# Performance work log

Hardware: AMD Instinct MI355X
Metric: run time of the kernel (lower is better)

Reference implementation:

```python
import jax, jax.numpy as jnp
import numpy as np

T, B, I, H = 512, 64, 256, 256
ACT_EXP2 = 7   # activation scale = 2^-7
W_EXP2 = 8     # weight scale = 2^-8
QMIN, QMAX = -128.0, 127.0  # int8 symmetric, zp=0


def fq(x, exp2_inv):
    """Fake-quantize (round/clamp/dequant) with straight-through estimator."""
    scale = 2.0 ** (-exp2_inv)
    y = jnp.clip(jnp.round(x / scale), QMIN, QMAX) * scale
    return x + jax.lax.stop_gradient(y - x)


def setup_inputs() -> dict:
    key = jax.random.key(0)
    k = jax.random.split(key, 5)
    x = jax.random.normal(k[0], (T, B, I), jnp.float32)
    h0 = jnp.zeros((B, H), jnp.float32)
    W = jax.random.normal(k[1], (I, 3 * H), jnp.float32) / np.sqrt(I)
    R = jax.random.normal(k[2], (H, 3 * H), jnp.float32) / np.sqrt(H)
    bx = jax.random.normal(k[3], (3 * H,), jnp.float32) * 0.1
    br = jax.random.normal(k[4], (3 * H,), jnp.float32) * 0.1
    return {"x": x, "h0": h0, "W": W, "R": R, "bx": bx, "br": br}


def gru_quant(x, h0, W, R, bx, br):
    # quantize weights/biases once (weight.W / weight.R / weight.bx / weight.br)
    Wq = fq(W, W_EXP2)
    Rq = fq(R, W_EXP2)
    bxq = fq(bx, W_EXP2)
    brq = fq(br, W_EXP2)
    # hoisted input matmul: Wx = fq(fq(x) @ Wq)  -> [T, B, 3H]
    Wx = fq(jnp.einsum('tbi,ij->tbj', fq(x, ACT_EXP2), Wq), ACT_EXP2)
    Hh = h0.shape[-1]
    bz, brg, bg = bxq[:Hh], bxq[Hh:2 * Hh], bxq[2 * Hh:]

    def step(h, wx_t):
        hq = fq(h, ACT_EXP2)                      # input.h
        Rh = fq(hq @ Rq, ACT_EXP2)                # matmul.Rh
        v = fq(Rh + brq, ACT_EXP2)                # op.Rh_add_br
        wz, wr, wg = wx_t[:, :Hh], wx_t[:, Hh:2 * Hh], wx_t[:, 2 * Hh:]
        vz, vr, vg = v[:, :Hh], v[:, Hh:2 * Hh], v[:, 2 * Hh:]
        z = fq(jax.nn.sigmoid(fq(wz + bz + vz, ACT_EXP2)), ACT_EXP2)  # gate.z
        r = fq(jax.nn.sigmoid(fq(wr + brg + vr, ACT_EXP2)), ACT_EXP2)  # gate.r
        rRh = fq(r * vg, ACT_EXP2)                # op.rRh
        g = fq(jnp.tanh(fq(wg + bg + rRh, ACT_EXP2)), ACT_EXP2)        # gate.g
        old = fq(z * h, ACT_EXP2)                 # op.old_contrib
        new = fq((1.0 - z) * g, ACT_EXP2)         # op.new_contrib
        h_new = old + new
        return h_new, h_new

    _, hs = jax.lax.scan(step, h0, Wx)  # hs: [T, B, H]
    return hs


def reference(x, h0, W, R, bx, br):
    return gru_quant(x, h0, W, R, bx, br)
```

## Files before the change

### kernel.cpp

```cpp
#include <hip/hip_runtime.h>
#include <hip/hip_bf16.h>
#include <stdint.h>


#define T_STEPS 512
#define BATCH   64
#define IDIM    256
#define HDIM    256
#define N3H     768

#if defined(__has_builtin)
#if __has_builtin(__builtin_amdgcn_sdot4)
#define DOT4(a,b,c) __builtin_amdgcn_sdot4((int)(a),(int)(b),(int)(c),false)
#endif
#endif
#ifndef DOT4
__device__ __forceinline__ int dot4_sw(uint32_t a, uint32_t b, int c){
  c += (int)(int8_t)(a)      * (int)(int8_t)(b);
  c += (int)(int8_t)(a>>8)   * (int)(int8_t)(b>>8);
  c += (int)(int8_t)(a>>16)  * (int)(int8_t)(b>>16);
  c += (int)(int8_t)(a>>24)  * (int)(int8_t)(b>>24);
  return c;
}
#define DOT4(a,b,c) dot4_sw((uint32_t)(a),(uint32_t)(b),(int)(c))
#endif

__device__ __forceinline__ int rneclamp(float v) {
  int q = (int)rintf(v);
  return min(127, max(-128, q));
}

__device__ __forceinline__ uint32_t packq4(float4 f, float sc) {
  uint32_t b0 = (uint32_t)(uint8_t)(int8_t)rneclamp(f.x * sc);
  uint32_t b1 = (uint32_t)(uint8_t)(int8_t)rneclamp(f.y * sc);
  uint32_t b2 = (uint32_t)(uint8_t)(int8_t)rneclamp(f.z * sc);
  uint32_t b3 = (uint32_t)(uint8_t)(int8_t)rneclamp(f.w * sc);
  return b0 | (b1 << 8) | (b2 << 16) | (b3 << 24);
}

__global__ void prep_kernel(const float* __restrict__ W, const float* __restrict__ R,
                            const float* __restrict__ bx, const float* __restrict__ br,
                            int8_t* __restrict__ Wq8cm, int8_t* __restrict__ Rq8cm,
                            int8_t* __restrict__ bx8, int8_t* __restrict__ br8) {
  const int NW = IDIM * N3H;
  int idx = blockIdx.x * 256 + threadIdx.x;
  if (idx < NW) {
    int k = idx / N3H, j = idx % N3H;
    Wq8cm[(size_t)j * IDIM + k] = (int8_t)rneclamp(W[idx] * 256.0f);
  } else if (idx < 2 * NW) {
    int i2 = idx - NW;
    int k = i2 / N3H, j = i2 % N3H;
    Rq8cm[(size_t)j * HDIM + k] = (int8_t)rneclamp(R[i2] * 256.0f);
  } else if (idx < 2 * NW + N3H) {
    int i2 = idx - 2 * NW;
    bx8[i2] = (int8_t)rneclamp(bx[i2] * 256.0f);
  } else if (idx < 2 * NW + 2 * N3H) {
    int i2 = idx - 2 * NW - N3H;
    br8[i2] = (int8_t)rneclamp(br[i2] * 256.0f);
  }
}

__global__ __launch_bounds__(768, 1) void gemm_wx_kernel(
    const float* __restrict__ x, const int8_t* __restrict__ Wq8cm,
    int8_t* __restrict__ WxQ8) {
  const int t = blockIdx.x;
  const int j = threadIdx.x;

  __shared__ uint4 xq4[64 * 16];
  uint32_t* xq = (uint32_t*)xq4;

  uint4 w[16];
  const uint4* wp = (const uint4*)(Wq8cm + (size_t)j * IDIM);
  #pragma unroll
  for (int kk = 0; kk < 16; ++kk) w[kk] = wp[kk];

  const float4* xg = (const float4*)(x) + (size_t)t * 4096;
  for (int i = j; i < 4096; i += 768) {
    float4 f = xg[i];
    xq[i] = packq4(f, 128.0f);
  }
  __syncthreads();

  for (int r = 0; r < 64; ++r) {
    int s = 0;
    #pragma unroll
    for (int kk = 0; kk < 16; ++kk) {
      uint4 hv = xq4[r * 16 + kk];
      s = DOT4(hv.x, w[kk].x, s);
      s = DOT4(hv.y, w[kk].y, s);
      s = DOT4(hv.z, w[kk].z, s);
      s = DOT4(hv.w, w[kk].w, s);
    }
    int q = rneclamp((float)s * (1.0f / 256.0f));
    WxQ8[((size_t)r * T_STEPS + t) * N3H + j] = (int8_t)q;
  }
}

__global__ __launch_bounds__(768, 1) void gru_rec_kernel(
    const float* __restrict__ h0, const int8_t* __restrict__ Rq8cm,
    const int8_t* __restrict__ bx8, const int8_t* __restrict__ br8,
    const int8_t* __restrict__ WxQ8, float* __restrict__ out) {
  const int b = blockIdx.x;
  const int j = threadIdx.x;

  __shared__ uint4 hq4[16];
  __shared__ int   v32[N3H];
  __shared__ int   wxs[N3H];
  __shared__ int8_t lutS[256];
  __shared__ int8_t lutT[256];

  uint4 w[16];
  const uint4* wp = (const uint4*)(Rq8cm + (size_t)j * HDIM);
  #pragma unroll
  for (int kk = 0; kk < 16; ++kk) w[kk] = wp[kk];
  const int brj = (int)br8[j];

  float hf = 0.0f;
  int bzc = 0, brc = 0, bgc = 0;
  if (j < HDIM) {
    hf  = h0[b * HDIM + j];
    bzc = (int)bx8[j];
    brc = (int)bx8[j + HDIM];
    bgc = (int)bx8[j + 2 * HDIM];
    double a = (double)(j - 128) / 128.0;
    lutS[j] = (int8_t)min(127, max(-128, (int)rint(128.0 / (1.0 + exp(-a)))));
    lutT[j] = (int8_t)min(127, max(-128, (int)rint(128.0 * tanh(a))));
    ((int8_t*)hq4)[j] = (int8_t)rneclamp(hf * 128.0f);
  }
  __syncthreads();

  const int8_t* wxp = WxQ8 + (size_t)b * T_STEPS * N3H + j;
  float* outp = out + (size_t)b * HDIM + (j < HDIM ? j : 0);

  for (int t = 0; t < T_STEPS; ++t) {
    int wxb = (int)wxp[(size_t)t * N3H];
    int s = 0;
    #pragma unroll
    for (int kk = 0; kk < 16; ++kk) {
      uint4 hv = hq4[kk];
      s = DOT4(hv.x, w[kk].x, s);
      s = DOT4(hv.y, w[kk].y, s);
      s = DOT4(hv.z, w[kk].z, s);
      s = DOT4(hv.w, w[kk].w, s);
    }
    int Rh = rneclamp((float)s * (1.0f / 256.0f));
    int v = rneclamp((float)(2 * Rh + brj) * 0.5f);
    v32[j] = v;
    wxs[j] = wxb;
    __syncthreads();

    if (j < HDIM) {
      int vz = v32[j], vr = v32[j + HDIM], vg = v32[j + 2 * HDIM];
      int wz = wxs[j], wr = wxs[j + HDIM], wg = wxs[j + 2 * HDIM];
      int az = rneclamp((float)(2 * wz + bzc + 2 * vz) * 0.5f);
      int zi = (int)lutS[az + 128];
      int ar = rneclamp((float)(2 * wr + brc + 2 * vr) * 0.5f);
      int ri = (int)lutS[ar + 128];
      int rrh = rneclamp((float)(ri * vg) * (1.0f / 128.0f));
      int ag = rneclamp((float)(2 * wg + bgc + 2 * rrh) * 0.5f);
      int gi = (int)lutT[ag + 128];
      int oldi = rneclamp((float)zi * hf);
      int newi = rneclamp((float)((128 - zi) * gi) * (1.0f / 128.0f));
      int hi = oldi + newi;
      hf = (float)hi * (1.0f / 128.0f);
      outp[(size_t)t * BATCH * HDIM] = hf;
      ((int8_t*)hq4)[j] = (int8_t)min(127, max(-128, hi));
    }
    __syncthreads();
  }
}

extern "C" void kernel_launch(void* const* d_in, const int* in_sizes, int n_in,
                              void* d_out, int out_size, void* d_ws, size_t ws_size,
                              hipStream_t stream) {
  const float* x  = (const float*)d_in[0];
  const float* h0 = (const float*)d_in[1];
  const float* W  = (const float*)d_in[2];
  const float* R  = (const float*)d_in[3];
  const float* bx = (const float*)d_in[4];
  const float* br = (const float*)d_in[5];
  float* out = (float*)d_out;

  const size_t NW = (size_t)IDIM * N3H;
  int8_t* Wq8cm = (int8_t*)d_ws;
  int8_t* Rq8cm = Wq8cm + NW;
  int8_t* bx8   = Rq8cm + NW;
  int8_t* br8   = bx8 + N3H;
  int8_t* WxQ8  = br8 + N3H;

  {
    int total = (int)(2 * NW + 2 * N3H);
    int blocks = (total + 255) / 256;
    prep_kernel<<<blocks, 256, 0, stream>>>(W, R, bx, br, Wq8cm, Rq8cm, bx8, br8);
  }
  gemm_wx_kernel<<<T_STEPS, 768, 0, stream>>>(x, Wq8cm, WxQ8);
  gru_rec_kernel<<<BATCH, 768, 0, stream>>>(h0, Rq8cm, bx8, br8, WxQ8, out);
}
```

Before: 544.7 us.

## Restructure GRU recurrence to one thread per hidden unit with readlane broadcast

The recurrent kernel now uses 256 threads per batch row, and each thread computes all three gate dot products for its hidden unit. It keeps 48 uint4 weight registers and broadcasts the packed hidden state through readlane instead of reading from LDS. This drops the intermediate v32/wxs shared-memory exchange and one barrier per step. The hidden state is double-buffered, the next step's Wx values are prefetched, and the weight layout changes to k-chunk-major so loads coalesce. The cost is high register pressure (192 VGPRs for weights) and three times the serial dot work per thread.

```diff
diff --git a/kernel.cpp b/kernel.cpp
--- a/kernel.cpp
+++ b/kernel.cpp
@@ -25,6 +25,9 @@
 #define DOT4(a,b,c) dot4_sw((uint32_t)(a),(uint32_t)(b),(int)(c))
 #endif
 
+#define CHUNK(W,c) (((c)&3)==0 ? W[(c)>>2].x : ((c)&3)==1 ? W[(c)>>2].y : \
+                    ((c)&3)==2 ? W[(c)>>2].z : W[(c)>>2].w)
+
 __device__ __forceinline__ int rneclamp(float v) {
   int q = (int)rintf(v);
   return min(127, max(-128, q));
@@ -40,17 +43,17 @@
 
 __global__ void prep_kernel(const float* __restrict__ W, const float* __restrict__ R,
                             const float* __restrict__ bx, const float* __restrict__ br,
-                            int8_t* __restrict__ Wq8cm, int8_t* __restrict__ Rq8cm,
+                            int8_t* __restrict__ Wq, int8_t* __restrict__ Rq,
                             int8_t* __restrict__ bx8, int8_t* __restrict__ br8) {
   const int NW = IDIM * N3H;
   int idx = blockIdx.x * 256 + threadIdx.x;
   if (idx < NW) {
     int k = idx / N3H, j = idx % N3H;
-    Wq8cm[(size_t)j * IDIM + k] = (int8_t)rneclamp(W[idx] * 256.0f);
+    Wq[((size_t)(k >> 4) * N3H + j) * 16 + (k & 15)] = (int8_t)rneclamp(W[idx] * 256.0f);
   } else if (idx < 2 * NW) {
     int i2 = idx - NW;
     int k = i2 / N3H, j = i2 % N3H;
-    Rq8cm[(size_t)j * HDIM + k] = (int8_t)rneclamp(R[i2] * 256.0f);
+    Rq[((size_t)(k >> 4) * N3H + j) * 16 + (k & 15)] = (int8_t)rneclamp(R[i2] * 256.0f);
   } else if (idx < 2 * NW + N3H) {
     int i2 = idx - 2 * NW;
     bx8[i2] = (int8_t)rneclamp(bx[i2] * 256.0f);
@@ -61,7 +64,7 @@
 }
 
 __global__ __launch_bounds__(768, 1) void gemm_wx_kernel(
-    const float* __restrict__ x, const int8_t* __restrict__ Wq8cm,
+    const float* __restrict__ x, const int8_t* __restrict__ Wq,
     int8_t* __restrict__ WxQ8) {
   const int t = blockIdx.x;
   const int j = threadIdx.x;
@@ -70,9 +73,9 @@
   uint32_t* xq = (uint32_t*)xq4;
 
   uint4 w[16];
-  const uint4* wp = (const uint4*)(Wq8cm + (size_t)j * IDIM);
+  const uint4* wp = (const uint4*)Wq;
   #pragma unroll
-  for (int kk = 0; kk < 16; ++kk) w[kk] = wp[kk];
+  for (int kk = 0; kk < 16; ++kk) w[kk] = wp[kk * N3H + j];
 
   const float4* xg = (const float4*)(x) + (size_t)t * 4096;
   for (int i = j; i < 4096; i += 768) {
@@ -96,77 +99,89 @@
   }
 }
 
-__global__ __launch_bounds__(768, 1) void gru_rec_kernel(
-    const float* __restrict__ h0, const int8_t* __restrict__ Rq8cm,
+__global__ __launch_bounds__(256, 1) void gru_rec2_kernel(
+    const float* __restrict__ h0, const int8_t* __restrict__ Rq,
     const int8_t* __restrict__ bx8, const int8_t* __restrict__ br8,
     const int8_t* __restrict__ WxQ8, float* __restrict__ out) {
   const int b = blockIdx.x;
   const int j = threadIdx.x;
-
-  __shared__ uint4 hq4[16];
-  __shared__ int   v32[N3H];
-  __shared__ int   wxs[N3H];
+  const int lane = j & 63;
+
+  __shared__ uint32_t hq[2][64];
   __shared__ int8_t lutS[256];
   __shared__ int8_t lutT[256];
 
-  uint4 w[16];
-  const uint4* wp = (const uint4*)(Rq8cm + (size_t)j * HDIM);
+  uint4 wz[16], wr[16], wg[16];
+  const uint4* rp = (const uint4*)Rq;
   #pragma unroll
-  for (int kk = 0; kk < 16; ++kk) w[kk] = wp[kk];
-  const int brj = (int)br8[j];
-
-  float hf = 0.0f;
-  int bzc = 0, brc = 0, bgc = 0;
-  if (j < HDIM) {
-    hf  = h0[b * HDIM + j];
-    bzc = (int)bx8[j];
-    brc = (int)bx8[j + HDIM];
-    bgc = (int)bx8[j + 2 * HDIM];
-    double a = (double)(j - 128) / 128.0;
+  for (int kk = 0; kk < 16; ++kk) {
+    wz[kk] = rp[kk * N3H + j];
+    wr[kk] = rp[kk * N3H + 256 + j];
+    wg[kk] = rp[kk * N3H + 512 + j];
+  }
+  const int bz  = (int)bx8[j];
+  const int brg = (int)bx8[j + 256];
+  const int bg  = (int)bx8[j + 512];
+  const int vbz = (int)br8[j];
+  const int vbr = (int)br8[j + 256];
+  const int vbg = (int)br8[j + 512];
+
+  {
+    double a = ((double)j - 128.0) / 128.0;
     lutS[j] = (int8_t)min(127, max(-128, (int)rint(128.0 / (1.0 + exp(-a)))));
     lutT[j] = (int8_t)min(127, max(-128, (int)rint(128.0 * tanh(a))));
-    ((int8_t*)hq4)[j] = (int8_t)rneclamp(hf * 128.0f);
-  }
+  }
+  float hf = h0[b * HDIM + j];
+  ((int8_t*)&hq[0][0])[j] = (int8_t)rneclamp(hf * 128.0f);
   __syncthreads();
 
   const int8_t* wxp = WxQ8 + (size_t)b * T_STEPS * N3H + j;
-  float* outp = out + (size_t)b * HDIM + (j < HDIM ? j : 0);
+  float* outp = out + (size_t)b * HDIM + j;
+
+  int wxz = (int)wxp[0];
+  int wxr = (int)wxp[256];
+  int wxg = (int)wxp[512];
 
   for (int t = 0; t < T_STEPS; ++t) {
-    int wxb = (int)wxp[(size_t)t * N3H];
-    int s = 0;
+    const int cur = t & 1, nxt = cur ^ 1;
+    int nz = 0, nr = 0, ng = 0;
+    if (t + 1 < T_STEPS) {
+      const int8_t* p = wxp + (size_t)(t + 1) * N3H;
+      nz = (int)p[0]; nr = (int)p[256]; ng = (int)p[512];
+    }
+
+    uint32_t hw = hq[cur][lane];
+    int sz = 0, sr = 0, sg = 0;
     #pragma unroll
-    for (int kk = 0; kk < 16; ++kk) {
-      uint4 hv = hq4[kk];
-      s = DOT4(hv.x, w[kk].x, s);
-      s = DOT4(hv.y, w[kk].y, s);
-      s = DOT4(hv.z, w[kk].z, s);
-      s = DOT4(hv.w, w[kk].w, s);
+    for (int c = 0; c < 64; ++c) {
+      int hc = __builtin_amdgcn_readlane((int)hw, c);
+      sz = DOT4(hc, CHUNK(wz, c), sz);
+      sr = DOT4(hc, CHUNK(wr, c), sr);
+      sg = DOT4(hc, CHUNK(wg, c), sg);
     }
-    int Rh = rneclamp((float)s * (1.0f / 256.0f));
-    int v = rneclamp((float)(2 * Rh + brj) * 0.5f);
-    v32[j] = v;
-    wxs[j] = wxb;
+    int Rz = rneclamp((float)sz * (1.0f / 256.0f));
+    int Rr = rneclamp((float)sr * (1.0f / 256.0f));
+    int Rg = rneclamp((float)sg * (1.0f / 256.0f));
+    int vz = rneclamp((float)(2 * Rz + vbz) * 0.5f);
+    int vr = rneclamp((float)(2 * Rr + vbr) * 0.5f);
+    int vg = rneclamp((float)(2 * Rg + vbg) * 0.5f);
+
+    int az = rneclamp((float)(2 * wxz + bz + 2 * vz) * 0.5f);
+    int zi = (int)lutS[az + 128];
+    int ar = rneclamp((float)(2 * wxr + brg + 2 * vr) * 0.5f);
+    int ri = (int)lutS[ar + 128];
+    int rrh = rneclamp((float)(ri * vg) * (1.0f / 128.0f));
+    int ag = rneclamp((float)(2 * wxg + bg + 2 * rrh) * 0.5f);
+    int gi = (int)lutT[ag + 128];
+    int oldi = rneclamp((float)zi * hf);
+    int newi = rneclamp((float)((128 - zi) * gi) * (1.0f / 128.0f));
+    int hi = oldi + newi;
+    hf = (float)hi * (1.0f / 128.0f);
+    outp[(size_t)t * BATCH * HDIM] = hf;
+    ((int8_t*)&hq[nxt][0])[j] = (int8_t)min(127, max(-128, hi));
     __syncthreads();
 
-    if (j < HDIM) {
-      int vz = v32[j], vr = v32[j + HDIM], vg = v32[j + 2 * HDIM];
-      int wz = wxs[j], wr = wxs[j + HDIM], wg = wxs[j + 2 * HDIM];
-      int az = rneclamp((float)(2 * wz + bzc + 2 * vz) * 0.5f);
-      int zi = (int)lutS[az + 128];
-      int ar = rneclamp((float)(2 * wr + brc + 2 * vr) * 0.5f);
-      int ri = (int)lutS[ar + 128];
-      int rrh = rneclamp((float)(ri * vg) * (1.0f / 128.0f));
-      int ag = rneclamp((float)(2 * wg + bgc + 2 * rrh) * 0.5f);
-      int gi = (int)lutT[ag + 128];
-      int oldi = rneclamp((float)zi * hf);
-      int newi = rneclamp((float)((128 - zi) * gi) * (1.0f / 128.0f));
-      int hi = oldi + newi;
-      hf = (float)hi * (1.0f / 128.0f);
-      outp[(size_t)t * BATCH * HDIM] = hf;
-      ((int8_t*)hq4)[j] = (int8_t)min(127, max(-128, hi));
-    }
-    __syncthreads();
+    wxz = nz; wxr = nr; wxg = ng;
   }
 }
 
@@ -182,17 +197,17 @@
   float* out = (float*)d_out;
 
   const size_t NW = (size_t)IDIM * N3H;
-  int8_t* Wq8cm = (int8_t*)d_ws;
-  int8_t* Rq8cm = Wq8cm + NW;
-  int8_t* bx8   = Rq8cm + NW;
-  int8_t* br8   = bx8 + N3H;
-  int8_t* WxQ8  = br8 + N3H;
+  int8_t* Wq  = (int8_t*)d_ws;
+  int8_t* Rq  = Wq + NW;
+  int8_t* bx8 = Rq + NW;
+  int8_t* br8 = bx8 + N3H;
+  int8_t* WxQ8 = br8 + N3H;
 
   {
     int total = (int)(2 * NW + 2 * N3H);
     int blocks = (total + 255) / 256;
-    prep_kernel<<<blocks, 256, 0, stream>>>(W, R, bx, br, Wq8cm, Rq8cm, bx8, br8);
-  }
-  gemm_wx_kernel<<<T_STEPS, 768, 0, stream>>>(x, Wq8cm, WxQ8);
-  gru_rec_kernel<<<BATCH, 768, 0, stream>>>(h0, Rq8cm, bx8, br8, WxQ8, out);
-}
+    prep_kernel<<<blocks, 256, 0, stream>>>(W, R, bx, br, Wq, Rq, bx8, br8);
+  }
+  gemm_wx_kernel<<<T_STEPS, 768, 0, stream>>>(x, Wq, WxQ8);
+  gru_rec2_kernel<<<BATCH, 256, 0, stream>>>(h0, Rq, bx8, br8, WxQ8, out);
+}
```

Result: faster. 488.8 us (-10.3%).
